# Performance work log

Hardware: AMD Instinct MI355X
Metric: run time of the kernel (lower is better)

The kernel has to match this reference:

```python
import jax, jax.numpy as jnp
import numpy as np

B, N, M, C, T, HF, WF = 4, 512, 32, 512, 8, 14, 14
K = 80          # num_classes
P = 7           # ROI pool output size
HID = 1024
IMG = 224


def setup_inputs() -> dict:
    key = jax.random.key(0)
    k0, k1, k2, k3, k4, k5 = jax.random.split(key, 6)
    feature = jax.random.normal(k0, (B, C, T, HF, WF), dtype=jnp.float32)
    # GT boxes: realistic xyxy boxes inside a 224x224 image
    ka, kb = jax.random.split(k1)
    cxy = jax.random.uniform(ka, (B, M, 2), minval=40.0, maxval=180.0)
    wh = jax.random.uniform(kb, (B, M, 2), minval=40.0, maxval=100.0)
    gt_bboxes = jnp.concatenate([cxy - wh / 2, cxy + wh / 2], axis=-1).astype(jnp.float32)
    # Proposals: jittered copies of GT boxes so many pass the IoU>=0.85 fg test
    idx = jnp.arange(N) % M
    base = gt_bboxes[:, idx]                                   # [B,N,4]
    noise = jax.random.normal(k2, (B, N, 4), dtype=jnp.float32) * 1.5
    proposal_bboxes = jnp.clip(base + noise, 0.0, float(IMG))
    gt_classes = (jax.random.uniform(k3, (B, M, K)) < 0.1).astype(jnp.float32)
    W1 = jax.random.normal(k4, (C * P * P, HID), dtype=jnp.float32) * 0.01
    b1 = jnp.zeros((HID,), jnp.float32)
    W2 = jax.random.normal(k5, (HID, K), dtype=jnp.float32) * 0.01
    b2 = jnp.zeros((K,), jnp.float32)
    return {"feature": feature, "proposal_bboxes": proposal_bboxes,
            "gt_bboxes": gt_bboxes, "gt_classes": gt_classes,
            "W1": W1, "b1": b1, "W2": W2, "b2": b2,
            "image_h": IMG, "image_w": IMG}


def _iou(a, b):
    # a [B,N,4], b [B,M,4] xyxy -> [B,N,M]
    lt = jnp.maximum(a[:, :, None, :2], b[:, None, :, :2])
    rb = jnp.minimum(a[:, :, None, 2:], b[:, None, :, 2:])
    wh = jnp.clip(rb - lt, 0.0)
    inter = wh[..., 0] * wh[..., 1]
    area_a = (a[..., 2] - a[..., 0]) * (a[..., 3] - a[..., 1])
    area_b = (b[..., 2] - b[..., 0]) * (b[..., 3] - b[..., 1])
    return inter / (area_a[:, :, None] + area_b[:, None, :] - inter + 1e-8)


def _roi_pool(feat_bhwc, boxes, bidx, sy, sx):
    # feat_bhwc [B,H,W,C]; boxes [R,4] image coords; bilinear 7x7 ROI pooling
    H, W = feat_bhwc.shape[1], feat_bhwc.shape[2]
    x1, y1, x2, y2 = boxes[:, 0] * sx, boxes[:, 1] * sy, boxes[:, 2] * sx, boxes[:, 3] * sy
    g = (jnp.arange(P, dtype=jnp.float32) + 0.5) / P
    ys = y1[:, None] + g[None, :] * (y2 - y1)[:, None]        # [R,P]
    xs = x1[:, None] + g[None, :] * (x2 - x1)[:, None]        # [R,P]
    y = jnp.broadcast_to(ys[:, :, None], (boxes.shape[0], P, P)) - 0.5
    x = jnp.broadcast_to(xs[:, None, :], (boxes.shape[0], P, P)) - 0.5
    y0f = jnp.floor(y); x0f = jnp.floor(x)
    wy = jnp.clip(y - y0f, 0.0, 1.0)[..., None]
    wx = jnp.clip(x - x0f, 0.0, 1.0)[..., None]
    y0 = jnp.clip(y0f, 0, H - 1).astype(jnp.int32)
    y1i = jnp.clip(y0f + 1, 0, H - 1).astype(jnp.int32)
    x0 = jnp.clip(x0f, 0, W - 1).astype(jnp.int32)
    x1i = jnp.clip(x0f + 1, 0, W - 1).astype(jnp.int32)
    bi = bidx[:, None, None]
    gather = lambda yy, xx: feat_bhwc[bi, yy, xx]             # [R,P,P,C]
    out = (gather(y0, x0) * (1 - wy) * (1 - wx) + gather(y0, x1i) * (1 - wy) * wx +
           gather(y1i, x0) * wy * (1 - wx) + gather(y1i, x1i) * wy * wx)
    return out


def reference(feature, proposal_bboxes, gt_bboxes, gt_classes, W1, b1, W2, b2, image_h, image_w):
    # temporal average pool (AvgPool3d over T) -> [B,C,HF,WF]
    feat = feature.mean(axis=2)
    feat_bhwc = jnp.transpose(feat, (0, 2, 3, 1))             # [B,HF,WF,C]
    # IoU-based fg assignment
    ious = _iou(proposal_bboxes, gt_bboxes)                   # [B,N,M]
    max_iou = ious.max(axis=2)                                # [B,N]
    assign = ious.argmax(axis=2)                              # [B,N]
    any_fg = jnp.any(max_iou >= 0.85)
    thresh = jnp.where(any_fg, 0.85, 0.5)                     # fallback branch
    fg = (max_iou >= thresh).astype(feature.dtype)            # [B,N]
    # ROI pool all proposals (bg masked out in the loss)
    boxes = proposal_bboxes.reshape(B * N, 4)
    bidx = jnp.repeat(jnp.arange(B, dtype=jnp.int32), N)
    sy = feat.shape[2] / float(image_h)
    sx = feat.shape[3] / float(image_w)
    pool = _roi_pool(feat_bhwc, boxes, bidx, sy, sx)          # [R,P,P,C]
    pool = jnp.transpose(pool, (0, 3, 1, 2)).reshape(B * N, C * P * P)
    hidden = jax.nn.relu(pool @ W1 + b1)                      # [R,HID]
    logits = hidden @ W2 + b2                                 # [R,K]
    # multilabel soft-margin labels per proposal
    labels = gt_classes[jnp.repeat(jnp.arange(B), N), assign.reshape(-1)]  # [R,K]
    per = -(labels * jax.nn.log_sigmoid(logits) +
            (1.0 - labels) * jax.nn.log_sigmoid(-logits)).mean(axis=-1)    # [R]
    per = per.reshape(B, N)
    cnt = fg.sum(axis=1)
    losses = jnp.where(cnt > 0, (per * fg).sum(axis=1) / jnp.maximum(cnt, 1.0), 0.0)
    return losses
```

## Files before the change

### kernel.cpp

```cpp
#include <hip/hip_runtime.h>
#include <cstdint>
#include <cstddef>

#define KTOT 25088
#define NBOX 2048
#define HID  1024

typedef __bf16 bf16x8 __attribute__((ext_vector_type(8)));
typedef float  f32x4  __attribute__((ext_vector_type(4)));

__device__ __forceinline__ unsigned short f2bf(float f) {
  union { float f; unsigned u; } v; v.f = f;
  unsigned r = v.u + 0x7FFFu + ((v.u >> 16) & 1u);
  return (unsigned short)(r >> 16);
}

__device__ __forceinline__ float scalar_f(const void* p) {
  int iv = *(const int*)p;
  if (iv > 0 && iv < (1 << 20)) return (float)iv;
  return *(const float*)p;
}

__global__ __launch_bounds__(256) void k_meant(const float* __restrict__ feature,
                                               float* __restrict__ fbhwc) {
  int id = blockIdx.x * 256 + threadIdx.x;
  if (id >= 4 * 512 * 196) return;
  int pix = id % 196;
  int c   = (id / 196) & 511;
  int b   = id / (196 * 512);
  const float* p = feature + ((size_t)(b * 512 + c) * 8) * 196 + pix;
  float s = 0.f;
#pragma unroll
  for (int t = 0; t < 8; ++t) s += p[t * 196];
  fbhwc[((size_t)(b * 196 + pix)) * 512 + c] = s * 0.125f;
}

__global__ __launch_bounds__(256) void k_iou(const float* __restrict__ prop,
                                             const float* __restrict__ gtb,
                                             float* __restrict__ max_iou,
                                             int* __restrict__ assign,
                                             int* __restrict__ flag) {
  __shared__ float g[128];
  int gid = blockIdx.x * 256 + threadIdx.x;
  int b = gid >> 9;
  if (threadIdx.x < 128) g[threadIdx.x] = gtb[b * 128 + threadIdx.x];
  __syncthreads();
  float x1 = prop[gid * 4 + 0], y1 = prop[gid * 4 + 1];
  float x2 = prop[gid * 4 + 2], y2 = prop[gid * 4 + 3];
  float aa = (x2 - x1) * (y2 - y1);
  float best = -1e30f; int arg = 0;
  for (int m = 0; m < 32; ++m) {
    float gx1 = g[m*4], gy1 = g[m*4+1], gx2 = g[m*4+2], gy2 = g[m*4+3];
    float iw = fmaxf(fminf(x2, gx2) - fmaxf(x1, gx1), 0.f);
    float ih = fmaxf(fminf(y2, gy2) - fmaxf(y1, gy1), 0.f);
    float inter = iw * ih;
    float ab = (gx2 - gx1) * (gy2 - gy1);
    float iou = inter / (aa + ab - inter + 1e-8f);
    if (iou > best) { best = iou; arg = m; }
  }
  max_iou[gid] = best; assign[gid] = arg;
  if (best >= 0.85f) atomicOr(flag, 1);
}

__global__ __launch_bounds__(256) void k_w1t(const float* __restrict__ W1,
                                             unsigned short* __restrict__ W1T) {
  __shared__ unsigned short tile[64][68];
  int kp0 = blockIdx.x * 64;
  int h0  = blockIdx.y * 64;
  int t = threadIdx.x;
  int seg = t & 15, ro = t >> 4;
#pragma unroll
  for (int r = 0; r < 4; ++r) {
    int i = ro + r * 16;
    int kp = kp0 + i;
    int srow = (kp & 511) * 49 + (kp >> 9);
    float4 v = *(const float4*)(W1 + (size_t)srow * 1024 + h0 + seg * 4);
    tile[i][seg*4+0] = f2bf(v.x);
    tile[i][seg*4+1] = f2bf(v.y);
    tile[i][seg*4+2] = f2bf(v.z);
    tile[i][seg*4+3] = f2bf(v.w);
  }
  __syncthreads();
#pragma unroll
  for (int r = 0; r < 4; ++r) {
    int hi = ro + r * 16;
    unsigned a = tile[seg*4+0][hi];
    unsigned b = tile[seg*4+1][hi];
    unsigned c = tile[seg*4+2][hi];
    unsigned d = tile[seg*4+3][hi];
    *(uint2*)(W1T + (size_t)(h0+hi)*KTOT + kp0 + seg*4) =
        make_uint2(a | (b << 16), c | (d << 16));
  }
}

__global__ __launch_bounds__(256) void k_roipool(const float* __restrict__ fbhwc,
                                                 const float* __restrict__ prop,
                                                 const void* ihp, const void* iwp,
                                                 unsigned short* __restrict__ Apool) {
  int n = blockIdx.x;
  int tid = threadIdx.x;
  float sy = 14.f / scalar_f(ihp);
  float sx = 14.f / scalar_f(iwp);
  float bx1 = prop[n*4+0]*sx, by1 = prop[n*4+1]*sy;
  float bx2 = prop[n*4+2]*sx, by2 = prop[n*4+3]*sy;
  const float* fb = fbhwc + (size_t)(n >> 9) * 196 * 512;
  unsigned short* arow = Apool + (size_t)n * KTOT;
  int c4 = (tid & 127) << 2;
  int bh = tid >> 7;
  for (int b2i = 0; b2i < 49; b2i += 2) {
    int bin = b2i + bh;
    if (bin >= 49) continue;
    int py = bin / 7, px = bin - py * 7;
    float y = by1 + ((py + 0.5f) * (1.f/7.f)) * (by2 - by1) - 0.5f;
    float x = bx1 + ((px + 0.5f) * (1.f/7.f)) * (bx2 - bx1) - 0.5f;
    float y0f = floorf(y), x0f = floorf(x);
    float wy = y - y0f, wx = x - x0f;
    int y0  = min(max((int)y0f, 0), 13);
    int y1i = min(max((int)y0f + 1, 0), 13);
    int x0  = min(max((int)x0f, 0), 13);
    int x1i = min(max((int)x0f + 1, 0), 13);
    float w00 = (1.f - wy) * (1.f - wx), w01 = (1.f - wy) * wx;
    float w10 = wy * (1.f - wx),         w11 = wy * wx;
    const float4 f00 = *(const float4*)(fb + (y0 * 14 + x0 ) * 512 + c4);
    const float4 f01 = *(const float4*)(fb + (y0 * 14 + x1i) * 512 + c4);
    const float4 f10 = *(const float4*)(fb + (y1i * 14 + x0 ) * 512 + c4);
    const float4 f11 = *(const float4*)(fb + (y1i * 14 + x1i) * 512 + c4);
    float vx = f00.x*w00 + f01.x*w01 + f10.x*w10 + f11.x*w11;
    float vy = f00.y*w00 + f01.y*w01 + f10.y*w10 + f11.y*w11;
    float vz = f00.z*w00 + f01.z*w01 + f10.z*w10 + f11.z*w11;
    float vw = f00.w*w00 + f01.w*w01 + f10.w*w10 + f11.w*w11;
    unsigned lo = (unsigned)f2bf(vx) | ((unsigned)f2bf(vy) << 16);
    unsigned hi = (unsigned)f2bf(vz) | ((unsigned)f2bf(vw) << 16);
    *(uint2*)(arow + bin * 512 + c4) = make_uint2(lo, hi);
  }
}

__device__ __forceinline__ void gload16(const unsigned short* g, unsigned short* l) {
  __builtin_amdgcn_global_load_lds(
      (const __attribute__((address_space(1))) unsigned int*)g,
      (__attribute__((address_space(3))) unsigned int*)l, 16, 0, 0);
}

__global__ __launch_bounds__(512, 2) void k_gemm1(
    const unsigned short* __restrict__ A,
    const unsigned short* __restrict__ B,
    unsigned short* __restrict__ hp)
{
  extern __shared__ unsigned short lds[];
  const int tid  = threadIdx.x;
  const int w    = tid >> 6;
  const int lane = tid & 63;
  const int l15  = lane & 15;
  const int wr = w >> 2, wc = w & 3;
  const int bid = (int)blockIdx.x;
  const int wg  = (bid & 7) * 32 + (bid >> 3);
  const int kb  = wg >> 5;
  const int gy  = (wg >> 2) & 7;
  const int gx  = wg & 3;

  f32x4 acc[8][4];
  const f32x4 zero = {0.f, 0.f, 0.f, 0.f};
#pragma unroll
  for (int m = 0; m < 8; ++m)
#pragma unroll
    for (int n = 0; n < 4; ++n) acc[m][n] = zero;

  const int xsw  = (tid & 7) ^ ((tid >> 3) & 7);
  const int rloc = ((tid >> 3) << 1) + (xsw >> 2);
  const int qsrc = xsw & 3;
  const size_t kbase = (size_t)kb * 3136;
  const unsigned short* gAp = A + (size_t)(gy * 256 + rloc) * KTOT + kbase + qsrc * 8;
  const unsigned short* gBp = B + (size_t)(gx * 256 + rloc) * KTOT + kbase + qsrc * 8;
  const int dstc = tid * 8;

  const int pfr   = ((lane >> 4) | ((l15 & 1) << 2)) ^ (l15 >> 1);
  const int aoffc = wr * 4096 + (l15 >> 1) * 64 + pfr * 8;
  const int boffc = wc * 2048 + (l15 >> 1) * 64 + pfr * 8;

  bf16x8 Afr[8], Bfr[4];

#define STG(SLOT, KN) { \
    gload16(gAp + (KN),                      lds + (SLOT)*16384 + dstc); \
    gload16(gAp + (KN) + (size_t)128 * KTOT, lds + (SLOT)*16384 + 4096 + dstc); \
    gload16(gBp + (KN),                      lds + (SLOT)*16384 + 8192 + dstc); \
    gload16(gBp + (KN) + (size_t)128 * KTOT, lds + (SLOT)*16384 + 12288 + dstc); }
#define LDA(i, SLOT) Afr[i] = *reinterpret_cast<const bf16x8*>( \
    lds + (SLOT)*16384 + aoffc + (i)*512);
#define LDB(n, SLOT) Bfr[n] = *reinterpret_cast<const bf16x8*>( \
    lds + (SLOT)*16384 + 8192 + boffc + (n)*512);
#define VM4 asm volatile("s_waitcnt vmcnt(4)" ::: "memory");
#define VM0 asm volatile("s_waitcnt vmcnt(0)" ::: "memory");
#define VMN

#define STEP(CS, DOSTG, KN, VMASM, DOREFILL)                                   \
  {                                                                            \
    if (DOSTG) STG((((CS)+2)&3), KN)                                           \
    VMASM                                                                      \
    __builtin_amdgcn_s_barrier();                                              \
    asm volatile("s_waitcnt lgkmcnt(0)" ::: "memory");                         \
    __builtin_amdgcn_sched_barrier(0);                                         \
    __builtin_amdgcn_s_setprio(1);                                             \
    _Pragma("unroll") for (int i = 0; i < 8; ++i) {                            \
      _Pragma("unroll") for (int n = 0; n < 4; ++n)                            \
        acc[i][n] = __builtin_amdgcn_mfma_f32_16x16x32_bf16(                   \
            Afr[i], Bfr[n], acc[i][n], 0, 0, 0);                               \
      if (DOREFILL) LDA(i, (((CS)+1)&3))                                       \
    }                                                                          \
    if (DOREFILL) { _Pragma("unroll") for (int n = 0; n < 4; ++n)              \
                      LDB(n, (((CS)+1)&3)) }                                   \
    __builtin_amdgcn_s_setprio(0);                                             \
    __builtin_amdgcn_sched_barrier(0);                                         \
  }

  STG(0, 0)
  STG(1, 32)
  VM4
  __builtin_amdgcn_s_barrier();
#pragma unroll
  for (int i = 0; i < 8; ++i) LDA(i, 0)
#pragma unroll
  for (int n = 0; n < 4; ++n) LDB(n, 0)

#pragma unroll 1
  for (int s4 = 0; s4 < 96; s4 += 4) {
    STEP(0, true, (size_t)(s4 + 2) * 32, VM4, true)
    STEP(1, true, (size_t)(s4 + 3) * 32, VM4, true)
    STEP(2, true, (size_t)(s4 + 4) * 32, VM4, true)
    STEP(3, true, (size_t)(s4 + 5) * 32, VM4, true)
  }
  STEP(0, false, 0, VM0, true)
  STEP(1, false, 0, VMN, false)

#undef STEP
#undef VMN
#undef VM0
#undef VM4
#undef LDB
#undef LDA
#undef STG

  unsigned short* o = hp + (size_t)kb * (2048u * 1024u);
  const int r0 = gy * 256 + wr * 128 + ((lane >> 4) << 2);
  const int c0 = gx * 256 + wc * 64 + l15;
#pragma unroll
  for (int m = 0; m < 8; ++m)
#pragma unroll
    for (int n = 0; n < 4; ++n)
#pragma unroll
      for (int j = 0; j < 4; ++j)
        o[(size_t)(r0 + m * 16 + j) * 1024 + c0 + n * 16] = f2bf(acc[m][n][j]);
}

template<int OUTBF>
__global__ __launch_bounds__(256, 4) void k_gemm(
    const unsigned short* __restrict__ A,
    const unsigned short* __restrict__ B,
    void* __restrict__ outp,
    int Kst, int kIters, int nTileBits, int mTileBits, int ldc)
{
  __shared__ unsigned short As[2][4096];
  __shared__ unsigned short Bs[2][4096];
  const int tid  = threadIdx.x;
  const int w    = tid >> 6;
  const int lane = tid & 63;
  const int nwg = (int)gridDim.x, cpx = nwg >> 3;
  const int bid = (int)blockIdx.x;
  const int wg  = (bid & 7) * cpx + (bid >> 3);
  const int kb  = wg >> (mTileBits + nTileBits);
  const int rem = wg & ((1 << (mTileBits + nTileBits)) - 1);
  const int gy  = rem >> nTileBits;
  const int gx  = rem & ((1 << nTileBits) - 1);
  const int wr = w >> 1, wc = w & 1;

  f32x4 acc[4][4];
  const f32x4 zero = {0.f, 0.f, 0.f, 0.f};
#pragma unroll
  for (int m = 0; m < 4; ++m)
#pragma unroll
    for (int n = 0; n < 4; ++n) acc[m][n] = zero;

  const int r0   = 32 * w + (lane >> 2);
  const int qsrc = (lane & 3) ^ ((lane >> 3) & 3);
  const size_t kbase = (size_t)kb * kIters * 32;
  const unsigned short* gA = A + (size_t)(gy * 128 + r0) * Kst + kbase + qsrc * 8;
  const unsigned short* gB = B + (size_t)(gx * 128 + r0) * Kst + kbase + qsrc * 8;
  const int ldst = r0 * 32 + (lane & 3) * 8;

  const int swq = ((lane >> 4) ^ ((lane >> 1) & 3)) * 8;
  const int ar = (wr * 64 + (lane & 15)) * 32 + swq;
  const int br = (wc * 64 + (lane & 15)) * 32 + swq;

#define STAGE(bufi, it) do {                                         \
    const unsigned short* pa = gA + (size_t)(it) * 32;               \
    const unsigned short* pb = gB + (size_t)(it) * 32;               \
    gload16(pa,                      &As[bufi][ldst]);               \
    gload16(pa + (size_t)16 * Kst,   &As[bufi][ldst + 512]);         \
    gload16(pb,                      &Bs[bufi][ldst]);               \
    gload16(pb + (size_t)16 * Kst,   &Bs[bufi][ldst + 512]);         \
  } while (0)

  STAGE(0, 0);
  int cur = 0;
  for (int kk = 0; kk < kIters; ++kk) {
    __syncthreads();
    if (kk + 1 < kIters) STAGE(cur ^ 1, kk + 1);
    bf16x8 af[4], bfr[4];
#pragma unroll
    for (int m = 0; m < 4; ++m)
      af[m] = *reinterpret_cast<const bf16x8*>(&As[cur][ar + m * 512]);
#pragma unroll
    for (int n = 0; n < 4; ++n)
      bfr[n] = *reinterpret_cast<const bf16x8*>(&Bs[cur][br + n * 512]);
#pragma unroll
    for (int m = 0; m < 4; ++m)
#pragma unroll
      for (int n = 0; n < 4; ++n)
        acc[m][n] = __builtin_amdgcn_mfma_f32_16x16x32_bf16(af[m], bfr[n], acc[m][n], 0, 0, 0);
    cur ^= 1;
  }
#undef STAGE

  const size_t M = (size_t)(1 << mTileBits) * 128;
  const size_t splitStride = M * (size_t)ldc;
  const int r0o = gy * 128 + wr * 64 + ((lane >> 4) << 2);
  const int c0o = gx * 128 + wc * 64 + (lane & 15);
  if (OUTBF) {
    unsigned short* o = (unsigned short*)outp + (size_t)kb * splitStride;
#pragma unroll
    for (int m = 0; m < 4; ++m)
#pragma unroll
      for (int n = 0; n < 4; ++n)
#pragma unroll
        for (int j = 0; j < 4; ++j)
          o[(size_t)(r0o + m * 16 + j) * ldc + c0o + n * 16] = f2bf(acc[m][n][j]);
  } else {
    float* o = (float*)outp + (size_t)kb * splitStride;
#pragma unroll
    for (int m = 0; m < 4; ++m)
#pragma unroll
      for (int n = 0; n < 4; ++n)
#pragma unroll
        for (int j = 0; j < 4; ++j)
          o[(size_t)(r0o + m * 16 + j) * ldc + c0o + n * 16] = acc[m][n][j];
  }
}

__global__ __launch_bounds__(256) void k_combine(const unsigned short* __restrict__ hp,
                                                 const float* __restrict__ b1,
                                                 unsigned short* __restrict__ hidden) {
  int gid = blockIdx.x * 256 + threadIdx.x;
  int id8 = gid * 8;
  int h = id8 & 1023;
  float a[8];
#pragma unroll
  for (int j = 0; j < 8; ++j) a[j] = b1[h + j];
#pragma unroll
  for (int s = 0; s < 8; ++s) {
    uint4 u = *(const uint4*)(hp + (size_t)s * 2097152 + id8);
    unsigned uu[4] = {u.x, u.y, u.z, u.w};
#pragma unroll
    for (int q = 0; q < 4; ++q) {
      union { unsigned u; float f; } lo, hi;
      lo.u = uu[q] << 16; hi.u = uu[q] & 0xFFFF0000u;
      a[2*q]   += lo.f;
      a[2*q+1] += hi.f;
    }
  }
  unsigned out[4];
#pragma unroll
  for (int q = 0; q < 4; ++q) {
    unsigned l  = f2bf(fmaxf(a[2*q],   0.f));
    unsigned hh = f2bf(fmaxf(a[2*q+1], 0.f));
    out[q] = l | (hh << 16);
  }
  *(uint4*)(hidden + id8) = make_uint4(out[0], out[1], out[2], out[3]);
}

__global__ __launch_bounds__(256) void k_w2t(const float* __restrict__ W2,
                                             unsigned short* __restrict__ W2T) {
  int id = blockIdx.x * 256 + threadIdx.x;
  int cls = id >> 10, k = id & 1023;
  float v = (cls < 80) ? W2[(size_t)k * 80 + cls] : 0.f;
  W2T[id] = f2bf(v);
}

__global__ __launch_bounds__(256) void k_bce(const float* __restrict__ hp2,
                                             const float* __restrict__ b2,
                                             const float* __restrict__ gtc,
                                             const int* __restrict__ assign,
                                             float* __restrict__ per) {
  __shared__ float red[256];
  int t = threadIdx.x;
  int box = t >> 4, li = t & 15;
  int n = blockIdx.x * 16 + box;
  int lab = ((n >> 9) * 32 + assign[n]) * 80;
  float s = 0.f;
#pragma unroll
  for (int j = 0; j < 5; ++j) {
    int c = li + 16 * j;
    size_t o = (size_t)n * 128 + c;
    float x = hp2[o] + hp2[o + 262144] + hp2[o + 524288] + hp2[o + 786432] + b2[c];
    float y = gtc[lab + c];
    float ce = log1pf(expf(-fabsf(x)));
    s += y * (fmaxf(-x, 0.f) + ce) + (1.f - y) * (fmaxf(x, 0.f) + ce);
  }
  red[t] = s;
  __syncthreads();
  if (li == 0) {
    float tot = 0.f;
#pragma unroll
    for (int i = 0; i < 16; ++i) tot += red[box * 16 + i];
    per[n] = tot * (1.f / 80.f);
  }
}

__global__ __launch_bounds__(512) void k_reduce(const float* __restrict__ per,
                                                const float* __restrict__ max_iou,
                                                const int* __restrict__ flag,
                                                float* __restrict__ out) {
  __shared__ float sv[8], sf[8];
  int b = blockIdx.x, tid = threadIdx.x;
  float thr = (*flag) ? 0.85f : 0.5f;
  int n = b * 512 + tid;
  float f = (max_iou[n] >= thr) ? 1.f : 0.f;
  float v = per[n] * f;
#pragma unroll
  for (int o = 32; o > 0; o >>= 1) {
    v += __shfl_down(v, o);
    f += __shfl_down(f, o);
  }
  int wv = tid >> 6;
  if ((tid & 63) == 0) { sv[wv] = v; sf[wv] = f; }
  __syncthreads();
  if (tid == 0) {
    float S = 0.f, F = 0.f;
#pragma unroll
    for (int i = 0; i < 8; ++i) { S += sv[i]; F += sf[i]; }
    out[b] = (F > 0.f) ? S / fmaxf(F, 1.f) : 0.f;
  }
}

extern "C" void kernel_launch(void* const* d_in, const int* in_sizes, int n_in,
                              void* d_out, int out_size, void* d_ws, size_t ws_size,
                              hipStream_t stream) {
  const float* feature = (const float*)d_in[0];
  const float* prop    = (const float*)d_in[1];
  const float* gtb     = (const float*)d_in[2];
  const float* gtc     = (const float*)d_in[3];
  const float* W1      = (const float*)d_in[4];
  const float* b1      = (const float*)d_in[5];
  const float* W2      = (const float*)d_in[6];
  const float* b2      = (const float*)d_in[7];
  const void*  ihp     = d_in[8];
  const void*  iwp     = d_in[9];

  char* ws = (char*)d_ws;
  float*          fbhwc  = (float*)(ws);
  unsigned short* W1T    = (unsigned short*)(ws + 1605632);
  unsigned short* Apool  = (unsigned short*)(ws + 52985856);
  unsigned short* hp     = (unsigned short*)(ws + 155746304);
  float*          max_iou= (float*)(ws + 189300736);
  int*            assign = (int*)(ws + 189308928);
  float*          per    = (float*)(ws + 189317120);
  int*            flag   = (int*)(ws + 189325312);
  unsigned short* hidden = W1T;
  unsigned short* W2T    = Apool;
  float*          hp2    = (float*)((char*)Apool + 262144);

  hipFuncSetAttribute((const void*)k_gemm1,
                      hipFuncAttributeMaxDynamicSharedMemorySize, 131072);

  hipMemsetAsync(flag, 0, sizeof(int), stream);
  k_meant  <<<1568, 256, 0, stream>>>(feature, fbhwc);
  k_iou    <<<8, 256, 0, stream>>>(prop, gtb, max_iou, assign, flag);
  k_w1t    <<<dim3(392, 16), 256, 0, stream>>>(W1, W1T);
  k_roipool<<<2048, 256, 0, stream>>>(fbhwc, prop, ihp, iwp, Apool);
  k_gemm1  <<<256, 512, 131072, stream>>>(Apool, W1T, hp);
  k_combine<<<1024, 256, 0, stream>>>(hp, b1, hidden);
  k_w2t    <<<512, 256, 0, stream>>>(W2, W2T);
  k_gemm<0><<<64, 256, 0, stream>>>(hidden, W2T, hp2, 1024, 8, 0, 4, 128);
  k_bce    <<<128, 256, 0, stream>>>(hp2, b2, gtc, assign, per);
  k_reduce <<<4, 512, 0, stream>>>(per, max_iou, flag, (float*)d_out);
}
```

Measured before the change: 200.2 us.

## Load A fragments directly from global memory in gemm1, staging only B through LDS

The split-K GEMM1 kernel no longer stages the A (pooled ROI) tile through LDS. Each wave now reads its A MFMA fragments straight from global memory one k-step ahead, while B keeps the 4-slot LDS ring. This halves LDS traffic and dynamic shared memory (131072 to 65536 bytes), which could allow more resident blocks. The cost is uncoalesced 16-byte strided global loads for A whose latency is hidden only by one step of lookahead, and vmcnt accounting that now mixes the direct A loads with the async B loads.

```diff
diff --git a/kernel.cpp b/kernel.cpp
--- a/kernel.cpp
+++ b/kernel.cpp
@@ -165,36 +165,35 @@
 #pragma unroll
     for (int n = 0; n < 4; ++n) acc[m][n] = zero;
 
+  const size_t kbase = (size_t)kb * 3136;
+
+  const unsigned short* gAf =
+      A + (size_t)(gy * 256 + wr * 128 + l15) * KTOT + kbase + (lane >> 4) * 8;
+
   const int xsw  = (tid & 7) ^ ((tid >> 3) & 7);
   const int rloc = ((tid >> 3) << 1) + (xsw >> 2);
   const int qsrc = xsw & 3;
-  const size_t kbase = (size_t)kb * 3136;
-  const unsigned short* gAp = A + (size_t)(gy * 256 + rloc) * KTOT + kbase + qsrc * 8;
   const unsigned short* gBp = B + (size_t)(gx * 256 + rloc) * KTOT + kbase + qsrc * 8;
   const int dstc = tid * 8;
 
   const int pfr   = ((lane >> 4) | ((l15 & 1) << 2)) ^ (l15 >> 1);
-  const int aoffc = wr * 4096 + (l15 >> 1) * 64 + pfr * 8;
   const int boffc = wc * 2048 + (l15 >> 1) * 64 + pfr * 8;
 
   bf16x8 Afr[8], Bfr[4];
 
-#define STG(SLOT, KN) { \
-    gload16(gAp + (KN),                      lds + (SLOT)*16384 + dstc); \
-    gload16(gAp + (KN) + (size_t)128 * KTOT, lds + (SLOT)*16384 + 4096 + dstc); \
-    gload16(gBp + (KN),                      lds + (SLOT)*16384 + 8192 + dstc); \
-    gload16(gBp + (KN) + (size_t)128 * KTOT, lds + (SLOT)*16384 + 12288 + dstc); }
-#define LDA(i, SLOT) Afr[i] = *reinterpret_cast<const bf16x8*>( \
-    lds + (SLOT)*16384 + aoffc + (i)*512);
+#define STGB(SLOT, KN) { \
+    gload16(gBp + (KN),                      lds + (SLOT)*8192 + dstc); \
+    gload16(gBp + (KN) + (size_t)128 * KTOT, lds + (SLOT)*8192 + 4096 + dstc); }
+#define LDA(i, KNA) Afr[i] = *reinterpret_cast<const bf16x8*>( \
+    gAf + (size_t)(i) * (16 * KTOT) + (KNA));
 #define LDB(n, SLOT) Bfr[n] = *reinterpret_cast<const bf16x8*>( \
-    lds + (SLOT)*16384 + 8192 + boffc + (n)*512);
-#define VM4 asm volatile("s_waitcnt vmcnt(4)" ::: "memory");
+    lds + (SLOT)*8192 + boffc + (n)*512);
+#define VM2 asm volatile("s_waitcnt vmcnt(2)" ::: "memory");
 #define VM0 asm volatile("s_waitcnt vmcnt(0)" ::: "memory");
-#define VMN
-
-#define STEP(CS, DOSTG, KN, VMASM, DOREFILL)                                   \
+
+#define STEP(CS, DOSTG, KNB, KNA, VMASM, DOREFILL)                             \
   {                                                                            \
-    if (DOSTG) STG((((CS)+2)&3), KN)                                           \
+    if (DOSTG) STGB((((CS)+2)&3), KNB)                                         \
     VMASM                                                                      \
     __builtin_amdgcn_s_barrier();                                              \
     asm volatile("s_waitcnt lgkmcnt(0)" ::: "memory");                         \
@@ -204,7 +203,7 @@
       _Pragma("unroll") for (int n = 0; n < 4; ++n)                            \
         acc[i][n] = __builtin_amdgcn_mfma_f32_16x16x32_bf16(                   \
             Afr[i], Bfr[n], acc[i][n], 0, 0, 0);                               \
-      if (DOREFILL) LDA(i, (((CS)+1)&3))                                       \
+      if (DOREFILL) LDA(i, KNA)                                                \
     }                                                                          \
     if (DOREFILL) { _Pragma("unroll") for (int n = 0; n < 4; ++n)              \
                       LDB(n, (((CS)+1)&3)) }                                   \
@@ -212,32 +211,32 @@
     __builtin_amdgcn_sched_barrier(0);                                         \
   }
 
-  STG(0, 0)
-  STG(1, 32)
-  VM4
+#pragma unroll
+  for (int i = 0; i < 8; ++i) LDA(i, 0)
+  __builtin_amdgcn_sched_barrier(0);
+  STGB(0, 0)
+  STGB(1, 32)
+  VM2
   __builtin_amdgcn_s_barrier();
-#pragma unroll
-  for (int i = 0; i < 8; ++i) LDA(i, 0)
 #pragma unroll
   for (int n = 0; n < 4; ++n) LDB(n, 0)
 
 #pragma unroll 1
   for (int s4 = 0; s4 < 96; s4 += 4) {
-    STEP(0, true, (size_t)(s4 + 2) * 32, VM4, true)
-    STEP(1, true, (size_t)(s4 + 3) * 32, VM4, true)
-    STEP(2, true, (size_t)(s4 + 4) * 32, VM4, true)
-    STEP(3, true, (size_t)(s4 + 5) * 32, VM4, true)
-  }
-  STEP(0, false, 0, VM0, true)
-  STEP(1, false, 0, VMN, false)
+    STEP(0, true, (size_t)(s4 + 2) * 32, (size_t)(s4 + 1) * 32, VM2, true)
+    STEP(1, true, (size_t)(s4 + 3) * 32, (size_t)(s4 + 2) * 32, VM2, true)
+    STEP(2, true, (size_t)(s4 + 4) * 32, (size_t)(s4 + 3) * 32, VM2, true)
+    STEP(3, true, (size_t)(s4 + 5) * 32, (size_t)(s4 + 4) * 32, VM2, true)
+  }
+  STEP(0, false, 0, (size_t)97 * 32, VM0, true)
+  STEP(1, false, 0, 0, VM0, false)
 
 #undef STEP
-#undef VMN
 #undef VM0
-#undef VM4
+#undef VM2
 #undef LDB
 #undef LDA
-#undef STG
+#undef STGB
 
   unsigned short* o = hp + (size_t)kb * (2048u * 1024u);
   const int r0 = gy * 256 + wr * 128 + ((lane >> 4) << 2);
@@ -468,14 +467,14 @@
   float*          hp2    = (float*)((char*)Apool + 262144);
 
   hipFuncSetAttribute((const void*)k_gemm1,
-                      hipFuncAttributeMaxDynamicSharedMemorySize, 131072);
+                      hipFuncAttributeMaxDynamicSharedMemorySize, 65536);
 
   hipMemsetAsync(flag, 0, sizeof(int), stream);
   k_meant  <<<1568, 256, 0, stream>>>(feature, fbhwc);
   k_iou    <<<8, 256, 0, stream>>>(prop, gtb, max_iou, assign, flag);
   k_w1t    <<<dim3(392, 16), 256, 0, stream>>>(W1, W1T);
   k_roipool<<<2048, 256, 0, stream>>>(fbhwc, prop, ihp, iwp, Apool);
-  k_gemm1  <<<256, 512, 131072, stream>>>(Apool, W1T, hp);
+  k_gemm1  <<<256, 512, 65536, stream>>>(Apool, W1T, hp);
   k_combine<<<1024, 256, 0, stream>>>(hp, b1, hidden);
   k_w2t    <<<512, 256, 0, stream>>>(W2, W2T);
   k_gemm<0><<<64, 256, 0, stream>>>(hidden, W2T, hp2, 1024, 8, 0, 4, 128);
```

Measured after the change: 318.5 us. +59.0%, slower.
